# Kernel tuning notes

Hardware: AMD Instinct MI355X
Metric: run time of the kernel (lower is better)

Reference implementation:

```python
import jax, jax.numpy as jnp
import numpy as np

HID = 256      # hidden_dim
EXPAND = 2
D_INNER = HID * EXPAND
LN_EPS = 1e-5


def _gru(xs, W_ih, W_hh, b_ih, b_hh):
    """torch nn.GRU (batch_first) over axis 1. xs: (N, P, d_inner) -> (N, P, H).
    Gate order (torch): r, z, n."""
    N = xs.shape[0]
    Hd = W_hh.shape[0]
    gi = xs @ W_ih + b_ih                 # (N, P, 3H) - input gates precomputed
    gi = jnp.swapaxes(gi, 0, 1)           # (P, N, 3H) for scan over P
    h0 = jnp.zeros((N, Hd), xs.dtype)

    def step(h, gi_t):
        gh = h @ W_hh + b_hh              # (N, 3H)
        ir, iz, i_n = jnp.split(gi_t, 3, axis=-1)
        hr, hz, h_n = jnp.split(gh, 3, axis=-1)
        r = jax.nn.sigmoid(ir + hr)
        z = jax.nn.sigmoid(iz + hz)
        n = jnp.tanh(i_n + r * h_n)
        h = (1.0 - z) * n + z * h
        return h, h

    _, ys = jax.lax.scan(step, h0, gi)    # (P, N, H)
    return jnp.swapaxes(ys, 0, 1)


def _branch(x2d, lin_W, lin_b, W_ih, W_hh, b_ih, b_hh):
    # Linear -> exact GELU (torch nn.GELU default) -> GRU
    h = jax.nn.gelu(x2d @ lin_W + lin_b, approximate=False)
    return _gru(h, W_ih, W_hh, b_ih, b_hh)


def setup_inputs() -> dict:
    key = jax.random.key(0)
    ks = jax.random.split(key, 16)
    s = 0.05
    p = {
        "x": jax.random.normal(ks[0], (8, 16, 1024, HID), jnp.float32),
        "fwd_lin_W": jax.random.normal(ks[1], (HID, D_INNER)) * s,
        "fwd_lin_b": jnp.zeros((D_INNER,)),
        "fwd_W_ih": jax.random.normal(ks[2], (D_INNER, 3 * HID)) * s,
        "fwd_W_hh": jax.random.normal(ks[3], (HID, 3 * HID)) * s,
        "fwd_b_ih": jnp.zeros((3 * HID,)),
        "fwd_b_hh": jnp.zeros((3 * HID,)),
        "bwd_lin_W": jax.random.normal(ks[4], (HID, D_INNER)) * s,
        "bwd_lin_b": jnp.zeros((D_INNER,)),
        "bwd_W_ih": jax.random.normal(ks[5], (D_INNER, 3 * HID)) * s,
        "bwd_W_hh": jax.random.normal(ks[6], (HID, 3 * HID)) * s,
        "bwd_b_ih": jnp.zeros((3 * HID,)),
        "bwd_b_hh": jnp.zeros((3 * HID,)),
        "proj_W": jax.random.normal(ks[7], (2 * HID, HID)) * s,
        "proj_b": jnp.zeros((HID,)),
        "ln_g": jnp.ones((HID,)),
        "ln_b": jnp.zeros((HID,)),
    }
    return p


def reference(x, fwd_lin_W, fwd_lin_b, fwd_W_ih, fwd_W_hh, fwd_b_ih, fwd_b_hh,
              bwd_lin_W, bwd_lin_b, bwd_W_ih, bwd_W_hh, bwd_b_ih, bwd_b_hh,
              proj_W, proj_b, ln_g, ln_b):
    B, T, P, H = x.shape
    xf = x.reshape(B * T, P, H)  # every timestep gets the identical spatial pass
    f_out = _branch(xf, fwd_lin_W, fwd_lin_b, fwd_W_ih, fwd_W_hh, fwd_b_ih, fwd_b_hh)
    b_out = _branch(xf[:, ::-1], bwd_lin_W, bwd_lin_b, bwd_W_ih, bwd_W_hh, bwd_b_ih, bwd_b_hh)[:, ::-1]
    cat = jnp.concatenate([f_out, b_out], axis=-1)          # (BT, P, 2H)
    out = cat @ proj_W + proj_b                              # (BT, P, H)
    out = out.reshape(B, T, P, H) + x                        # residual
    mu = out.mean(-1, keepdims=True)
    var = out.var(-1, keepdims=True)
    return (out - mu) * jax.lax.rsqrt(var + LN_EPS) * ln_g + ln_b
```

## Files before the change

kernel.cpp:

```cpp
#include <hip/hip_runtime.h>
#include <cmath>


typedef _Float16 h8  __attribute__((ext_vector_type(8)));
typedef _Float16 h2v __attribute__((ext_vector_type(2)));
typedef float    f32x4 __attribute__((ext_vector_type(4)));

#define MTOT 131072L
#define PSEQ 1024

__device__ __forceinline__ void dot2_asm(float& acc, unsigned int a, unsigned int b) {
    asm("v_dot2_f32_f16 %0, %1, %2, %0" : "+v"(acc) : "v"(a), "v"(b));
}

__device__ __forceinline__ float fast_sigmoid(float x) {
    float e = __builtin_amdgcn_exp2f(-1.44269504089f * x);
    return __builtin_amdgcn_rcpf(1.f + e);
}
__device__ __forceinline__ float fast_tanh(float x) {
    float e = __builtin_amdgcn_exp2f(-2.88539008178f * x);
    return (1.f - e) * __builtin_amdgcn_rcpf(1.f + e);
}

template <int MODE>
__global__ __launch_bounds__(256) void k_gemm(
    const void* __restrict__ Aa_, const void* __restrict__ Ab_,
    const float* __restrict__ B, const float* __restrict__ bias,
    const float* __restrict__ xres, void* __restrict__ out_)
{
    constexpr int K = (MODE == 0) ? 256 : 512;
    constexpr int N = (MODE == 0) ? 512 : (MODE == 1 ? 768 : 256);

    __shared__ __align__(16) _Float16 Al[64][40];
    __shared__ __align__(16) _Float16 Bl[64][40];

    const int tid  = threadIdx.x;
    const int lane = tid & 63;
    const int wave = tid >> 6;
    const int wm = wave >> 1, wn = wave & 1;
    const long bm0 = (long)blockIdx.x * 64;
    const int  bn0 = blockIdx.y * 64;

    const int sm  = tid >> 2;
    const int ska = (tid & 3) * 8;
    const int sn  = tid & 63;
    const int skb = (tid >> 6) * 8;

    f32x4 acc[2][2] = {};

    for (int kt = 0; kt < K / 32; ++kt) {
        h8 av;
        if constexpr (MODE == 0) {
            const float* ap = (const float*)Aa_ + (bm0 + sm) * 256 + kt * 32 + ska;
            #pragma unroll
            for (int i = 0; i < 8; ++i) av[i] = (_Float16)ap[i];
        } else if constexpr (MODE == 1) {
            av = *(const h8*)((const _Float16*)Aa_ + (bm0 + sm) * 512 + kt * 32 + ska);
        } else {
            const _Float16* src = (kt < 8) ? (const _Float16*)Aa_ : (const _Float16*)Ab_;
            av = *(const h8*)(src + (bm0 + sm) * 256 + (kt & 7) * 32 + ska);
        }
        *(h8*)&Al[sm][ska] = av;

        h8 bv;
        #pragma unroll
        for (int i = 0; i < 8; ++i)
            bv[i] = (_Float16)B[(long)(kt * 32 + skb + i) * N + bn0 + sn];
        *(h8*)&Bl[sn][skb] = bv;

        __syncthreads();

        const int fr = lane & 15, fg = lane >> 4;
        h8 a0 = *(const h8*)&Al[wm * 32 +      fr][fg * 8];
        h8 a1 = *(const h8*)&Al[wm * 32 + 16 + fr][fg * 8];
        h8 b0 = *(const h8*)&Bl[wn * 32 +      fr][fg * 8];
        h8 b1 = *(const h8*)&Bl[wn * 32 + 16 + fr][fg * 8];
        acc[0][0] = __builtin_amdgcn_mfma_f32_16x16x32_f16(a0, b0, acc[0][0], 0, 0, 0);
        acc[0][1] = __builtin_amdgcn_mfma_f32_16x16x32_f16(a0, b1, acc[0][1], 0, 0, 0);
        acc[1][0] = __builtin_amdgcn_mfma_f32_16x16x32_f16(a1, b0, acc[1][0], 0, 0, 0);
        acc[1][1] = __builtin_amdgcn_mfma_f32_16x16x32_f16(a1, b1, acc[1][1], 0, 0, 0);

        __syncthreads();
    }

    const int fr = lane & 15, fg = lane >> 4;
    #pragma unroll
    for (int fm = 0; fm < 2; ++fm)
    #pragma unroll
    for (int fn = 0; fn < 2; ++fn)
    #pragma unroll
    for (int r = 0; r < 4; ++r) {
        long row = bm0 + wm * 32 + fm * 16 + fg * 4 + r;
        int  col = bn0 + wn * 32 + fn * 16 + fr;
        float v = acc[fm][fn][r] + bias[col];
        if constexpr (MODE == 0) {
            v = 0.5f * v * (1.0f + erff(v * 0.70710678118654752f));
            ((_Float16*)out_)[row * (long)N + col] = (_Float16)v;
        } else if constexpr (MODE == 1) {
            ((_Float16*)out_)[row * (long)N + col] = (_Float16)v;
        } else {
            v += xres[row * 256 + col];
            ((float*)out_)[row * 256 + col] = v;
        }
    }
}

__global__ __launch_bounds__(256) void k_prep(
    const float* __restrict__ Whh, _Float16* __restrict__ Wp)
{
    const int t = blockIdx.x * 256 + threadIdx.x;
    const int j = t % 768, kk = t / 768;
    h2v v;
    v[0] = (_Float16)Whh[(2 * kk) * 768 + j];
    v[1] = (_Float16)Whh[(2 * kk + 1) * 768 + j];
    *(h2v*)(Wp + (long)j * 256 + 2 * kk) = v;
}

__global__ __launch_bounds__(768) __attribute__((amdgpu_waves_per_eu(3, 3)))
void k_gru(
    const _Float16* __restrict__ gif, const _Float16* __restrict__ gib,
    const _Float16* __restrict__ Wpf, const _Float16* __restrict__ Wpb,
    const float* __restrict__ bhhf, const float* __restrict__ bhhb,
    _Float16* __restrict__ hof, _Float16* __restrict__ hob)
{
    const int bid = blockIdx.x;
    const int branch = bid & 1;
    const int seq = bid >> 1;
    const int j = threadIdx.x;

    const _Float16* gi = (branch ? gib : gif) + (long)seq * PSEQ * 768;
    const _Float16* Wp = branch ? Wpb : Wpf;
    const float* bhh = branch ? bhhb : bhhf;
    _Float16* ho = (branch ? hob : hof) + (long)seq * PSEQ * 256;

    unsigned int w[128];
    const uint4* wsrc = (const uint4*)(Wp + (long)j * 256);
    #pragma unroll
    for (int i = 0; i < 32; ++i) {
        uint4 t = wsrc[i];
        w[4 * i + 0] = t.x;
        w[4 * i + 1] = t.y;
        w[4 * i + 2] = t.z;
        w[4 * i + 3] = t.w;
    }
    #pragma unroll
    for (int kk = 0; kk < 128; ++kk)
        asm volatile("" : "+v"(w[kk]));
    const float bj = bhh[j];

    __shared__ __align__(16) _Float16 sh_h[256];
    __shared__ float a_lds[768];
    __shared__ float gin_lds[256];

    if (j < 256) sh_h[j] = (_Float16)0.f;
    __syncthreads();

    const int dir = branch ? -1 : 1;
    int p = branch ? (PSEQ - 1) : 0;
    float gcur = (float)gi[(long)p * 768 + j];
    float hu = 0.f;

    for (int step = 0; step < PSEQ; ++step) {
        float gnxt = 0.f;
        if (step < PSEQ - 1) gnxt = (float)gi[(long)(p + dir) * 768 + j];

        float acc0 = 0.f, acc1 = 0.f, acc2 = 0.f, acc3 = 0.f;
        const uint4* h4 = (const uint4*)sh_h;
        #pragma unroll
        for (int i = 0; i < 32; ++i) {
            uint4 hv = h4[i];
            dot2_asm(acc0, w[4 * i + 0], hv.x);
            dot2_asm(acc1, w[4 * i + 1], hv.y);
            dot2_asm(acc2, w[4 * i + 2], hv.z);
            dot2_asm(acc3, w[4 * i + 3], hv.w);
        }
        float gh = (acc0 + acc1) + (acc2 + acc3) + bj;

        if (j < 512) { a_lds[j] = gcur + gh; }
        else         { a_lds[j] = gh; gin_lds[j - 512] = gcur; }
        __syncthreads();

        if (j < 256) {
            float r = fast_sigmoid(a_lds[j]);
            float z = fast_sigmoid(a_lds[256 + j]);
            float n = fast_tanh(gin_lds[j] + r * a_lds[512 + j]);
            hu = fmaf(z, hu - n, n);
            sh_h[j] = (_Float16)hu;
            ho[(long)p * 256 + j] = (_Float16)hu;
        }
        __syncthreads();

        gcur = gnxt;
        p += dir;
    }
}

__global__ __launch_bounds__(256) void k_ln(
    const float* __restrict__ pre, const float* __restrict__ g,
    const float* __restrict__ b, float* __restrict__ out)
{
    const long row = (long)blockIdx.x * 4 + (threadIdx.x >> 6);
    const int lane = threadIdx.x & 63;
    const float4 v = *(const float4*)&pre[row * 256 + lane * 4];
    float s  = v.x + v.y + v.z + v.w;
    float s2 = v.x * v.x + v.y * v.y + v.z * v.z + v.w * v.w;
    #pragma unroll
    for (int off = 32; off > 0; off >>= 1) {
        s  += __shfl_xor(s, off);
        s2 += __shfl_xor(s2, off);
    }
    const float mu  = s * (1.f / 256.f);
    const float var = s2 * (1.f / 256.f) - mu * mu;
    const float inv = rsqrtf(var + 1e-5f);
    const float4 gg = *(const float4*)&g[lane * 4];
    const float4 bb = *(const float4*)&b[lane * 4];
    float4 o;
    o.x = (v.x - mu) * inv * gg.x + bb.x;
    o.y = (v.y - mu) * inv * gg.y + bb.y;
    o.z = (v.z - mu) * inv * gg.z + bb.z;
    o.w = (v.w - mu) * inv * gg.w + bb.w;
    *(float4*)&out[row * 256 + lane * 4] = o;
}

extern "C" void kernel_launch(void* const* d_in, const int* in_sizes, int n_in,
                              void* d_out, int out_size, void* d_ws, size_t ws_size,
                              hipStream_t stream)
{
    const float* x       = (const float*)d_in[0];
    const float* f_lin_W = (const float*)d_in[1];
    const float* f_lin_b = (const float*)d_in[2];
    const float* f_W_ih  = (const float*)d_in[3];
    const float* f_W_hh  = (const float*)d_in[4];
    const float* f_b_ih  = (const float*)d_in[5];
    const float* f_b_hh  = (const float*)d_in[6];
    const float* b_lin_W = (const float*)d_in[7];
    const float* b_lin_b = (const float*)d_in[8];
    const float* b_W_ih  = (const float*)d_in[9];
    const float* b_W_hh  = (const float*)d_in[10];
    const float* b_b_ih  = (const float*)d_in[11];
    const float* b_b_hh  = (const float*)d_in[12];
    const float* proj_W  = (const float*)d_in[13];
    const float* proj_b  = (const float*)d_in[14];
    const float* ln_g    = (const float*)d_in[15];
    const float* ln_bb   = (const float*)d_in[16];

    char* ws = (char*)d_ws;

    const size_t BASE   = 1 << 20;
    const size_t GI_PER = (size_t)MTOT * 768 * 2;
    const size_t H1_OFF = BASE + 2 * GI_PER;
    const size_t H1_FULL = (size_t)MTOT * 512 * 2 * 2;
    int chunks = (ws_size >= H1_OFF + H1_FULL) ? 1
               : (ws_size >= H1_OFF + H1_FULL / 4) ? 4 : 8;
    const long MC = MTOT / chunks;

    _Float16* wpf = (_Float16*)ws;
    _Float16* wpb = (_Float16*)(ws + (512 << 10));
    _Float16* gif = (_Float16*)(ws + BASE);
    _Float16* gib = (_Float16*)(ws + BASE + GI_PER);
    float*    pre = (float*)(ws + BASE);
    _Float16* h1f = (_Float16*)(ws + H1_OFF);
    _Float16* h1b = h1f + MC * 512;

    _Float16* hof = (_Float16*)d_out;
    _Float16* hob = hof + MTOT * 256;

    k_prep<<<384, 256, 0, stream>>>(f_W_hh, wpf);
    k_prep<<<384, 256, 0, stream>>>(b_W_hh, wpb);

    for (int c = 0; c < chunks; ++c) {
        const long r0 = c * MC;
        k_gemm<0><<<dim3(MC / 64, 8),  256, 0, stream>>>(x + r0 * 256, nullptr, f_lin_W, f_lin_b, nullptr, h1f);
        k_gemm<0><<<dim3(MC / 64, 8),  256, 0, stream>>>(x + r0 * 256, nullptr, b_lin_W, b_lin_b, nullptr, h1b);
        k_gemm<1><<<dim3(MC / 64, 12), 256, 0, stream>>>(h1f, nullptr, f_W_ih, f_b_ih, nullptr, gif + r0 * 768);
        k_gemm<1><<<dim3(MC / 64, 12), 256, 0, stream>>>(h1b, nullptr, b_W_ih, b_b_ih, nullptr, gib + r0 * 768);
    }
    k_gru<<<256, 768, 0, stream>>>(gif, gib, wpf, wpb, f_b_hh, b_b_hh, hof, hob);
    k_gemm<2><<<dim3(MTOT / 64, 4), 256, 0, stream>>>(hof, hob, proj_W, proj_b, x, pre);
    k_ln<<<MTOT / 4, 256, 0, stream>>>(pre, ln_g, ln_bb, (float*)d_out);
}
```

Baseline: 2.457 ms.

## Batch 16 GRU sequences per block with MFMA recurrent matmul

Replaces the per-sequence dot2 GRU kernel with one that processes 16 sequences per block. The recurrent h@W_hh is done with 16x16x32 f16 MFMA: the r/z weight fragments sit in registers and the n-gate weights in LDS, and the hidden state is double-buffered in LDS. The input-gate GEMM now writes its output directly in a fragment-friendly layout matching the new kernel. The r/z hidden biases are folded into the input bias by a small prep kernel. The GRU launch drops from 256 blocks to 16, so far fewer CUs are used, but the redundant per-step work across sequences is removed.

```diff
diff --git a/kernel.cpp b/kernel.cpp
--- a/kernel.cpp
+++ b/kernel.cpp
@@ -8,10 +8,6 @@
 
 #define MTOT 131072L
 #define PSEQ 1024
-
-__device__ __forceinline__ void dot2_asm(float& acc, unsigned int a, unsigned int b) {
-    asm("v_dot2_f32_f16 %0, %1, %2, %0" : "+v"(acc) : "v"(a), "v"(b));
-}
 
 __device__ __forceinline__ float fast_sigmoid(float x) {
     float e = __builtin_amdgcn_exp2f(-1.44269504089f * x);
@@ -26,7 +22,7 @@
 __global__ __launch_bounds__(256) void k_gemm(
     const void* __restrict__ Aa_, const void* __restrict__ Ab_,
     const float* __restrict__ B, const float* __restrict__ bias,
-    const float* __restrict__ xres, void* __restrict__ out_)
+    const float* __restrict__ xres, void* __restrict__ out_, long m_off)
 {
     constexpr int K = (MODE == 0) ? 256 : 512;
     constexpr int N = (MODE == 0) ? 512 : (MODE == 1 ? 768 : 256);
@@ -38,8 +34,8 @@
     const int lane = tid & 63;
     const int wave = tid >> 6;
     const int wm = wave >> 1, wn = wave & 1;
-    const long bm0 = (long)blockIdx.x * 64;
-    const int  bn0 = blockIdx.y * 64;
+    const long bm0 = (long)(MODE == 1 ? blockIdx.y : blockIdx.x) * 64;
+    const int  bn0 = (MODE == 1 ? blockIdx.x : blockIdx.y) * 64;
 
     const int sm  = tid >> 2;
     const int ska = (tid & 3) * 8;
@@ -97,7 +93,15 @@
             v = 0.5f * v * (1.0f + erff(v * 0.70710678118654752f));
             ((_Float16*)out_)[row * (long)N + col] = (_Float16)v;
         } else if constexpr (MODE == 1) {
-            ((_Float16*)out_)[row * (long)N + col] = (_Float16)v;
+            long grow = row + m_off;
+            int seq = (int)(grow >> 10), p = (int)(grow & 1023);
+            int blk = seq >> 4, srow = seq & 15;
+            int g = col >> 8, ci = col & 255;
+            int wv = ci >> 5, tp = (ci >> 4) & 1;
+            int ln = (ci & 15) | ((srow >> 2) << 4);
+            int e = tp * 4 + (srow & 3);
+            long oidx = (((long)(blk * 1024 + p) * 3 + g) * 512 + (wv * 64 + ln)) * 8 + e;
+            ((_Float16*)out_)[oidx] = (_Float16)v;
         } else {
             v += xres[row * 256 + col];
             ((float*)out_)[row * 256 + col] = v;
@@ -105,93 +109,123 @@
     }
 }
 
-__global__ __launch_bounds__(256) void k_prep(
+__global__ __launch_bounds__(256) void k_prep_frag(
     const float* __restrict__ Whh, _Float16* __restrict__ Wp)
 {
     const int t = blockIdx.x * 256 + threadIdx.x;
-    const int j = t % 768, kk = t / 768;
-    h2v v;
-    v[0] = (_Float16)Whh[(2 * kk) * 768 + j];
-    v[1] = (_Float16)Whh[(2 * kk + 1) * 768 + j];
-    *(h2v*)(Wp + (long)j * 256 + 2 * kk) = v;
-}
-
-__global__ __launch_bounds__(768) __attribute__((amdgpu_waves_per_eu(3, 3)))
-void k_gru(
-    const _Float16* __restrict__ gif, const _Float16* __restrict__ gib,
+    const int l = t & 63, f = t >> 6;
+    const int kt = f & 7;
+    const int q  = f >> 3;
+    const int tp = q & 1;
+    const int q2 = q >> 1;
+    const int g  = q2 % 3, w = q2 / 3;
+    const int col = g * 256 + w * 32 + tp * 16 + (l & 15);
+    const int k0  = kt * 32 + (l >> 4) * 8;
+    h8 v;
+    #pragma unroll
+    for (int i = 0; i < 8; ++i)
+        v[i] = (_Float16)Whh[(long)(k0 + i) * 768 + col];
+    ((h8*)Wp)[t] = v;
+}
+
+__global__ __launch_bounds__(256) void k_prep_bias(
+    const float* __restrict__ bih, const float* __restrict__ bhh, float* __restrict__ bc)
+{
+    const int c = blockIdx.x * 256 + threadIdx.x;
+    bc[c] = bih[c] + (c < 512 ? bhh[c] : 0.f);
+}
+
+__global__ __launch_bounds__(512, 2) void k_gru2(
+    const _Float16* __restrict__ gpf, const _Float16* __restrict__ gpb,
     const _Float16* __restrict__ Wpf, const _Float16* __restrict__ Wpb,
     const float* __restrict__ bhhf, const float* __restrict__ bhhb,
     _Float16* __restrict__ hof, _Float16* __restrict__ hob)
 {
-    const int bid = blockIdx.x;
-    const int branch = bid & 1;
-    const int seq = bid >> 1;
-    const int j = threadIdx.x;
-
-    const _Float16* gi = (branch ? gib : gif) + (long)seq * PSEQ * 768;
-    const _Float16* Wp = branch ? Wpb : Wpf;
-    const float* bhh = branch ? bhhb : bhhf;
-    _Float16* ho = (branch ? hob : hof) + (long)seq * PSEQ * 256;
-
-    unsigned int w[128];
-    const uint4* wsrc = (const uint4*)(Wp + (long)j * 256);
-    #pragma unroll
-    for (int i = 0; i < 32; ++i) {
-        uint4 t = wsrc[i];
-        w[4 * i + 0] = t.x;
-        w[4 * i + 1] = t.y;
-        w[4 * i + 2] = t.z;
-        w[4 * i + 3] = t.w;
-    }
-    #pragma unroll
-    for (int kk = 0; kk < 128; ++kk)
-        asm volatile("" : "+v"(w[kk]));
-    const float bj = bhh[j];
-
-    __shared__ __align__(16) _Float16 sh_h[256];
-    __shared__ float a_lds[768];
-    __shared__ float gin_lds[256];
-
-    if (j < 256) sh_h[j] = (_Float16)0.f;
+    const int b = blockIdx.x;
+    const int dir = b & 1;
+    const int blk = b >> 1;
+    const int t = threadIdx.x;
+    const int w = t >> 6, l = t & 63;
+    const int lr = l & 15, lq = l >> 4;
+
+    const _Float16* gp  = dir ? gpb : gpf;
+    const _Float16* Wp  = dir ? Wpb : Wpf;
+    const float*    bhh = dir ? bhhb : bhhf;
+    _Float16*       hoo = dir ? hob : hof;
+
+    __shared__ __align__(16) h8 wn_lds[8192];
+    __shared__ __align__(16) _Float16 hbuf[2][16][264];
+
+    h8 bfrz[2][2][8];
+    {
+        const h8* src = (const h8*)Wp + (long)w * 48 * 64 + l;
+        #pragma unroll
+        for (int g = 0; g < 2; ++g)
+        #pragma unroll
+        for (int tp = 0; tp < 2; ++tp)
+        #pragma unroll
+        for (int kt = 0; kt < 8; ++kt)
+            bfrz[g][tp][kt] = src[((g * 2 + tp) * 8 + kt) * 64];
+        #pragma unroll
+        for (int tp = 0; tp < 2; ++tp)
+        #pragma unroll
+        for (int kt = 0; kt < 8; ++kt)
+            wn_lds[((w * 2 + tp) * 8 + kt) * 64 + l] = src[((4 + tp) * 8 + kt) * 64];
+    }
+    const int col0 = w * 32 + lr;
+    const float bn0 = bhh[512 + col0];
+    const float bn1 = bhh[512 + col0 + 16];
+
+    for (int i = t; i < 2 * 16 * 264; i += 512) ((_Float16*)hbuf)[i] = (_Float16)0.f;
     __syncthreads();
 
-    const int dir = branch ? -1 : 1;
-    int p = branch ? (PSEQ - 1) : 0;
-    float gcur = (float)gi[(long)p * 768 + j];
-    float hu = 0.f;
+    const int d = dir ? -1 : 1;
+    int p = dir ? (PSEQ - 1) : 0;
+    int cur = 0;
+    const long tbase = (long)t * 8;
+    const long bbase = (long)blk * 1024;
+    float hold[2][4] = {};
 
     for (int step = 0; step < PSEQ; ++step) {
-        float gnxt = 0.f;
-        if (step < PSEQ - 1) gnxt = (float)gi[(long)(p + dir) * 768 + j];
-
-        float acc0 = 0.f, acc1 = 0.f, acc2 = 0.f, acc3 = 0.f;
-        const uint4* h4 = (const uint4*)sh_h;
-        #pragma unroll
-        for (int i = 0; i < 32; ++i) {
-            uint4 hv = h4[i];
-            dot2_asm(acc0, w[4 * i + 0], hv.x);
-            dot2_asm(acc1, w[4 * i + 1], hv.y);
-            dot2_asm(acc2, w[4 * i + 2], hv.z);
-            dot2_asm(acc3, w[4 * i + 3], hv.w);
+        h8 gv0 = *(const h8*)(gp + ((bbase + p) * 3 + 0) * 4096 + tbase);
+        h8 gv1 = *(const h8*)(gp + ((bbase + p) * 3 + 1) * 4096 + tbase);
+        h8 gv2 = *(const h8*)(gp + ((bbase + p) * 3 + 2) * 4096 + tbase);
+
+        f32x4 acc[3][2] = {};
+        #pragma unroll
+        for (int kt = 0; kt < 8; ++kt) {
+            h8 af = *(const h8*)&hbuf[cur][lr][kt * 32 + lq * 8];
+            #pragma unroll
+            for (int tp = 0; tp < 2; ++tp) {
+                acc[0][tp] = __builtin_amdgcn_mfma_f32_16x16x32_f16(af, bfrz[0][tp][kt], acc[0][tp], 0, 0, 0);
+                acc[1][tp] = __builtin_amdgcn_mfma_f32_16x16x32_f16(af, bfrz[1][tp][kt], acc[1][tp], 0, 0, 0);
+                h8 bfn = wn_lds[((w * 2 + tp) * 8 + kt) * 64 + l];
+                acc[2][tp] = __builtin_amdgcn_mfma_f32_16x16x32_f16(af, bfn, acc[2][tp], 0, 0, 0);
+            }
         }
-        float gh = (acc0 + acc1) + (acc2 + acc3) + bj;
-
-        if (j < 512) { a_lds[j] = gcur + gh; }
-        else         { a_lds[j] = gh; gin_lds[j - 512] = gcur; }
-        __syncthreads();
-
-        if (j < 256) {
-            float r = fast_sigmoid(a_lds[j]);
-            float z = fast_sigmoid(a_lds[256 + j]);
-            float n = fast_tanh(gin_lds[j] + r * a_lds[512 + j]);
-            hu = fmaf(z, hu - n, n);
-            sh_h[j] = (_Float16)hu;
-            ho[(long)p * 256 + j] = (_Float16)hu;
+
+        #pragma unroll
+        for (int tp = 0; tp < 2; ++tp) {
+            const int col = col0 + tp * 16;
+            const float bn = tp ? bn1 : bn0;
+            #pragma unroll
+            for (int r = 0; r < 4; ++r) {
+                const int e = tp * 4 + r;
+                float rr = fast_sigmoid(acc[0][tp][r] + (float)gv0[e]);
+                float zz = fast_sigmoid(acc[1][tp][r] + (float)gv1[e]);
+                float nh = acc[2][tp][r] + bn;
+                float nn = fast_tanh((float)gv2[e] + rr * nh);
+                float h  = fmaf(zz, hold[tp][r] - nn, nn);
+                hold[tp][r] = h;
+                _Float16 hf = (_Float16)h;
+                const int row = lq * 4 + r;
+                hbuf[cur ^ 1][row][col] = hf;
+                hoo[((long)(blk * 16 + row) * PSEQ + p) * 256 + col] = hf;
+            }
         }
         __syncthreads();
 
-        gcur = gnxt;
-        p += dir;
+        cur ^= 1; p += d;
     }
 }
 
@@ -255,7 +289,9 @@
     const long MC = MTOT / chunks;
 
     _Float16* wpf = (_Float16*)ws;
-    _Float16* wpb = (_Float16*)(ws + (512 << 10));
+    _Float16* wpb = (_Float16*)(ws + 393216);
+    float*    bcf = (float*)(ws + 786432);
+    float*    bcb = (float*)(ws + 786432 + 3072);
     _Float16* gif = (_Float16*)(ws + BASE);
     _Float16* gib = (_Float16*)(ws + BASE + GI_PER);
     float*    pre = (float*)(ws + BASE);
@@ -265,17 +301,19 @@
     _Float16* hof = (_Float16*)d_out;
     _Float16* hob = hof + MTOT * 256;
 
-    k_prep<<<384, 256, 0, stream>>>(f_W_hh, wpf);
-    k_prep<<<384, 256, 0, stream>>>(b_W_hh, wpb);
+    k_prep_frag<<<96, 256, 0, stream>>>(f_W_hh, wpf);
+    k_prep_frag<<<96, 256, 0, stream>>>(b_W_hh, wpb);
+    k_prep_bias<<<3, 256, 0, stream>>>(f_b_ih, f_b_hh, bcf);
+    k_prep_bias<<<3, 256, 0, stream>>>(b_b_ih, b_b_hh, bcb);
 
     for (int c = 0; c < chunks; ++c) {
         const long r0 = c * MC;
-        k_gemm<0><<<dim3(MC / 64, 8),  256, 0, stream>>>(x + r0 * 256, nullptr, f_lin_W, f_lin_b, nullptr, h1f);
-        k_gemm<0><<<dim3(MC / 64, 8),  256, 0, stream>>>(x + r0 * 256, nullptr, b_lin_W, b_lin_b, nullptr, h1b);
-        k_gemm<1><<<dim3(MC / 64, 12), 256, 0, stream>>>(h1f, nullptr, f_W_ih, f_b_ih, nullptr, gif + r0 * 768);
-        k_gemm<1><<<dim3(MC / 64, 12), 256, 0, stream>>>(h1b, nullptr, b_W_ih, b_b_ih, nullptr, gib + r0 * 768);
-    }
-    k_gru<<<256, 768, 0, stream>>>(gif, gib, wpf, wpb, f_b_hh, b_b_hh, hof, hob);
-    k_gemm<2><<<dim3(MTOT / 64, 4), 256, 0, stream>>>(hof, hob, proj_W, proj_b, x, pre);
+        k_gemm<0><<<dim3(MC / 64, 8),  256, 0, stream>>>(x + r0 * 256, nullptr, f_lin_W, f_lin_b, nullptr, h1f, 0L);
+        k_gemm<0><<<dim3(MC / 64, 8),  256, 0, stream>>>(x + r0 * 256, nullptr, b_lin_W, b_lin_b, nullptr, h1b, 0L);
+        k_gemm<1><<<dim3(12, MC / 64), 256, 0, stream>>>(h1f, nullptr, f_W_ih, bcf, nullptr, gif, r0);
+        k_gemm<1><<<dim3(12, MC / 64), 256, 0, stream>>>(h1b, nullptr, b_W_ih, bcb, nullptr, gib, r0);
+    }
+    k_gru2<<<16, 512, 0, stream>>>(gif, gib, wpf, wpb, f_b_hh, b_b_hh, hof, hob);
+    k_gemm<2><<<dim3(MTOT / 64, 4), 256, 0, stream>>>(hof, hob, proj_W, proj_b, x, pre, 0L);
     k_ln<<<MTOT / 4, 256, 0, stream>>>(pre, ln_g, ln_bb, (float*)d_out);
 }
```

New measurement: 3.292 ms. +34.0%, slower.
